# Optimization experiments

Hardware: AMD Instinct MI355X
Metric: run time of the kernel (lower is better)

The kernel has to match this reference:

```python
import jax, jax.numpy as jnp
import numpy as np

LAMDA = 0.5
BATCH_SIZE = 1024
MARGIN = 0.5
NEG_OFFSET = 100000.0
INTRA_MARGIN = 0.1
EPS = 1e-12


def setup_inputs() -> dict:
    key = jax.random.key(0)
    k1, k2, k3 = jax.random.split(key, 3)
    feat = jax.random.normal(k1, (2 * BATCH_SIZE, 128), dtype=jnp.float32)
    label1 = jax.random.randint(k2, (BATCH_SIZE,), 0, 128, dtype=jnp.int64)
    label2 = jax.random.randint(k3, (BATCH_SIZE,), 0, 128, dtype=jnp.int64)
    return {"feat": feat, "label1": label1, "label2": label2}


def _cdist(a, b):
    # faithful to source: broadcasted diff, sqrt(sum(d^2) + 1e-12)
    diffs = a[:, None, :] - b[None, :, :]          # [N, M, D]
    return jnp.sqrt(jnp.sum(diffs * diffs, axis=-1) + EPS)


def _half(f_a, f_b, lab_a, lab_b, f_intra, margin):
    dis = _cdist(f_a, f_b)                          # [B, B]
    s = (lab_a[:, None] == lab_b[None, :]).astype(dis.dtype)
    furthest_positive = jnp.max(dis * s, axis=1)
    pos_positive = jnp.argmax(dis * s, axis=1)
    closest_negative = jnp.min(dis + NEG_OFFSET * s, axis=1)
    pos_negative = jnp.argmin(dis + NEG_OFFSET * s, axis=1)
    cross = jnp.mean(jnp.clip(furthest_positive - closest_negative + margin, 0.0))
    dis_intra = _cdist(f_intra, f_intra)            # [B, B]
    gathered = dis_intra[pos_positive, pos_negative]  # gather_2d equivalent
    intra = jnp.mean(jnp.clip(INTRA_MARGIN - gathered, 0.0))
    return cross, intra


def reference(feat, label1, label2):
    feature1 = feat[:BATCH_SIZE]
    feature2 = feat[BATCH_SIZE:]
    cross1, intra1 = _half(feature1, feature2, label1, label2, feature2, MARGIN)
    cross2, intra2 = _half(feature2, feature1, label2, label1, feature1, MARGIN)
    return (cross1 + cross2) + LAMDA * (intra1 + intra2)
```

## Files before the change

### kernel.cpp

```cpp
#include <hip/hip_runtime.h>
#include <math.h>
#include <float.h>

#define BATCH 1024
#define DIM 128
#define EPSV 1e-12f
#define MARGIN 0.5f
#define INTRA_MARGIN 0.1f
#define LAMDA 0.5f

typedef __attribute__((ext_vector_type(8))) short s16x8;
typedef __attribute__((ext_vector_type(4))) float f32x4;

__device__ __forceinline__ ushort f2bf(float f) {
    unsigned u = __float_as_uint(f);
    return (ushort)((u + 0x7fffu + ((u >> 16) & 1u)) >> 16);
}

__device__ __forceinline__ void gl_lds16(const void* g, void* l) {
    __builtin_amdgcn_global_load_lds(
        (const __attribute__((address_space(1))) unsigned int*)g,
        (__attribute__((address_space(3))) unsigned int*)l,
        16, 0, 0);
}

#define WAITVM4()  do { asm volatile("s_waitcnt vmcnt(4)" ::: "memory"); __builtin_amdgcn_sched_barrier(0); } while (0)
#define WAITVM0()  do { asm volatile("s_waitcnt vmcnt(0)" ::: "memory"); __builtin_amdgcn_sched_barrier(0); } while (0)
#define WAITLGKM() do { asm volatile("s_waitcnt lgkmcnt(0)" ::: "memory"); __builtin_amdgcn_sched_barrier(0); } while (0)

__global__ __launch_bounds__(256) void prep_kernel(
    const float* __restrict__ feat, ushort* __restrict__ bhi,
    float* __restrict__ norm2)
{
    const int t = threadIdx.x;
    const int gt  = blockIdx.x * 256 + t;
    const int row = gt >> 4, seg = gt & 15;
    const float4* p = reinterpret_cast<const float4*>(feat + (size_t)row * DIM + seg * 8);
    const float4 a = p[0], b = p[1];
    const float v[8] = {a.x, a.y, a.z, a.w, b.x, b.y, b.z, b.w};
    ushort h[8];
    float n = 0.0f;
    #pragma unroll
    for (int e = 0; e < 8; ++e) {
        h[e] = f2bf(v[e]);
        n = fmaf(v[e], v[e], n);
    }
    uint4 uh;
    uh.x = (uint)h[0] | ((uint)h[1] << 16); uh.y = (uint)h[2] | ((uint)h[3] << 16);
    uh.z = (uint)h[4] | ((uint)h[5] << 16); uh.w = (uint)h[6] | ((uint)h[7] << 16);
    reinterpret_cast<uint4*>(bhi)[row * 16 + (seg ^ (row & 7))] = uh;
    n += __shfl_xor(n, 1); n += __shfl_xor(n, 2);
    n += __shfl_xor(n, 4); n += __shfl_xor(n, 8);
    if ((t & 15) == 0) norm2[row] = n;
}

__device__ __forceinline__ void issue_chunk(const char* bbytes, size_t gbase,
                                            char* buf, int w, int lane) {
    #pragma unroll
    for (int i = 0; i < 4; ++i) {
        const int o = w * 4096 + i * 1024 + lane * 16;
        gl_lds16(bbytes + gbase + o, buf + o);
    }
}

__global__ __launch_bounds__(512, 2) void gemm_kernel(
    const ushort* __restrict__ bhi, const float* __restrict__ norm2,
    const float* __restrict__ feat,
    const int* __restrict__ label1, const int* __restrict__ label2,
    float* __restrict__ partial)
{
    __shared__ __align__(16) char smem[65536];

    const int rg    = blockIdx.x;
    const int half  = rg >> 7;
    const int arow0 = (rg & 127) * 8;
    const int aglob0 = half * BATCH + arow0;
    const int bglob0 = (half ^ 1) * BATCH;

    const int t = threadIdx.x;
    const int w = t >> 6, lane = t & 63;
    const int l15 = lane & 15, kg = lane >> 4;

    const int* labA = half ? label2 : label1;
    const int* labB = half ? label1 : label2;

    float nb[8]; int lb[8];
    #pragma unroll
    for (int c = 0; c < 8; ++c) {
        const int jc = c * 128 + w * 16 + l15;
        nb[c] = norm2[bglob0 + jc];
        lb[c] = labB[jc];
    }
    float na[4]; int la[4];
    #pragma unroll
    for (int r = 0; r < 4; ++r) {
        const int rr = (kg * 4 + r) & 7;
        na[r] = norm2[aglob0 + rr];
        la[r] = labA[arow0 + rr];
    }

    s16x8 ah[4];
    const size_t abase = (size_t)(aglob0 + (l15 & 7)) * DIM;
    #pragma unroll
    for (int kt = 0; kt < 4; ++kt) {
        const int kh = (kt * 32 + kg * 8) ^ ((l15 & 7) << 3);
        ah[kt] = *reinterpret_cast<const s16x8*>(bhi + abase + kh);
    }

    const char* bbytes = reinterpret_cast<const char*>(bhi);
    char* buf0 = smem;
    char* buf1 = smem + 32768;
    issue_chunk(bbytes, (size_t)(bglob0 + 0 * 128) * 256, buf0, w, lane);
    issue_chunk(bbytes, (size_t)(bglob0 + 1 * 128) * 256, buf1, w, lane);
    WAITVM4();

    float bpv[4], bnv[4]; int bpj[4], bnj[4];
    #pragma unroll
    for (int r = 0; r < 4; ++r) { bpv[r] = -1.0f; bpj[r] = 0x7fffffff; bnv[r] = FLT_MAX; bnj[r] = 0x7fffffff; }

    const int jl = w * 16 + l15;
    const ushort* b0 = reinterpret_cast<const ushort*>(buf0);
    const ushort* b1 = reinterpret_cast<const ushort*>(buf1);

    #pragma unroll
    for (int c = 0; c < 8; ++c) {
        const ushort* bufc = (c & 1) ? b1 : b0;

        s16x8 bh[4];
        #pragma unroll
        for (int kt = 0; kt < 4; ++kt) {
            const int kh = (kt * 32 + kg * 8) ^ ((l15 & 7) << 3);
            bh[kt] = *reinterpret_cast<const s16x8*>(bufc + jl * DIM + kh);
        }
        if (c < 6) {
            WAITLGKM();
            issue_chunk(bbytes, (size_t)(bglob0 + (c + 2) * 128) * 256,
                        (c & 1) ? buf1 : buf0, w, lane);
        }

        f32x4 acc = (f32x4){0.f, 0.f, 0.f, 0.f};
        #pragma unroll
        for (int kt = 0; kt < 4; ++kt)
            acc = __builtin_amdgcn_mfma_f32_16x16x32_bf16(ah[kt], bh[kt], acc, 0, 0, 0);

        const int jc = c * 128 + jl;
        #pragma unroll
        for (int r = 0; r < 4; ++r) {
            const float d2 = fmaxf(na[r] + nb[c] - 2.0f * acc[r], 0.0f);
            const bool same = (la[r] == lb[c]);
            const float pv = same ? d2 : 0.0f;
            const float nv = same ? FLT_MAX : d2;
            if (pv > bpv[r]) { bpv[r] = pv; bpj[r] = jc; }
            if (nv < bnv[r]) { bnv[r] = nv; bnj[r] = jc; }
        }

        if (c < 6)      WAITVM4();
        else if (c == 6) WAITVM0();
    }

    #pragma unroll
    for (int r = 0; r < 4; ++r) {
        #pragma unroll
        for (int m = 8; m > 0; m >>= 1) {
            const float opv = __shfl_xor(bpv[r], m); const int opj = __shfl_xor(bpj[r], m);
            if (opv > bpv[r] || (opv == bpv[r] && opj < bpj[r])) { bpv[r] = opv; bpj[r] = opj; }
            const float onv = __shfl_xor(bnv[r], m); const int onj = __shfl_xor(bnj[r], m);
            if (onv < bnv[r] || (onv == bnv[r] && onj < bnj[r])) { bnv[r] = onv; bnj[r] = onj; }
        }
    }

    __syncthreads();

    float (*L_pv)[8] = (float(*)[8])(smem);
    int   (*L_pj)[8] = (int  (*)[8])(smem + 512);
    float (*L_nv)[8] = (float(*)[8])(smem + 1024);
    int   (*L_nj)[8] = (int  (*)[8])(smem + 1536);
    int*   s_pp = (int*)  (smem + 2048);
    int*   s_pn = (int*)  (smem + 2112);
    float* s_fp = (float*)(smem + 2176);
    float* s_cn = (float*)(smem + 2240);
    float* ls   = (float*)(smem + 2304);

    if (l15 == 0) {
        #pragma unroll
        for (int r = 0; r < 4; ++r) {
            const int rib = kg * 4 + r;
            L_pv[rib][w] = bpv[r]; L_pj[rib][w] = bpj[r];
            L_nv[rib][w] = bnv[r]; L_nj[rib][w] = bnj[r];
        }
    }
    __syncthreads();

    if (t < 8) {
        float pv = -1.0f; int pj = 0x7fffffff; float nv = FLT_MAX; int nj = 0x7fffffff;
        #pragma unroll
        for (int c = 0; c < 8; ++c) {
            const float v1 = L_pv[t][c]; const int j1 = L_pj[t][c];
            if (v1 > pv || (v1 == pv && j1 < pj)) { pv = v1; pj = j1; }
            const float v2 = L_nv[t][c]; const int j2 = L_nj[t][c];
            if (v2 < nv || (v2 == nv && j2 < nj)) { nv = v2; nj = j2; }
        }
        s_pp[t] = pj > (BATCH - 1) ? (BATCH - 1) : pj;
        s_pn[t] = nj > (BATCH - 1) ? (BATCH - 1) : nj;
        s_fp[t] = (pv > 0.0f) ? sqrtf(pv + EPSV) : 0.0f;
        s_cn[t] = sqrtf(nv + EPSV);
    }
    __syncthreads();

    if (t < 128) {
        const int g = t >> 4, sl = t & 15;
        const float* fB = feat + (size_t)(half ^ 1) * BATCH * DIM;
        const float4* x = reinterpret_cast<const float4*>(fB + (size_t)s_pp[g] * DIM + sl * 8);
        const float4* y = reinterpret_cast<const float4*>(fB + (size_t)s_pn[g] * DIM + sl * 8);
        const float4 x0 = x[0], x1 = x[1], y0 = y[0], y1 = y[1];
        float d, d2;
        d = x0.x - y0.x; d2  = d * d;  d = x0.y - y0.y; d2 += d * d;
        d = x0.z - y0.z; d2 += d * d;  d = x0.w - y0.w; d2 += d * d;
        d = x1.x - y1.x; d2 += d * d;  d = x1.y - y1.y; d2 += d * d;
        d = x1.z - y1.z; d2 += d * d;  d = x1.w - y1.w; d2 += d * d;
        d2 += __shfl_xor(d2, 1); d2 += __shfl_xor(d2, 2);
        d2 += __shfl_xor(d2, 4); d2 += __shfl_xor(d2, 8);
        if (sl == 0) {
            const float gd = sqrtf(d2 + EPSV);
            const float loss = fmaxf(s_fp[g] - s_cn[g] + MARGIN, 0.0f)
                             + LAMDA * fmaxf(INTRA_MARGIN - gd, 0.0f);
            ls[g] = loss * (1.0f / (float)BATCH);
        }
    }
    __syncthreads();

    if (t == 0) {
        float s = 0.0f;
        #pragma unroll
        for (int i = 0; i < 8; ++i) s += ls[i];
        partial[rg] = s;
    }
}

__global__ __launch_bounds__(256) void reduce_kernel(
    const float* __restrict__ partial, float* __restrict__ out)
{
    const int t = threadIdx.x;
    float s = partial[t];
    #pragma unroll
    for (int m = 32; m > 0; m >>= 1) s += __shfl_down(s, m);
    __shared__ float ws4[4];
    if ((t & 63) == 0) ws4[t >> 6] = s;
    __syncthreads();
    if (t == 0) out[0] = ws4[0] + ws4[1] + ws4[2] + ws4[3];
}

extern "C" void kernel_launch(void* const* d_in, const int* in_sizes, int n_in,
                              void* d_out, int out_size, void* d_ws, size_t ws_size,
                              hipStream_t stream) {
    const float* feat   = (const float*)d_in[0];
    const int*   label1 = (const int*)d_in[1];
    const int*   label2 = (const int*)d_in[2];
    float* out = (float*)d_out;

    char* ws = (char*)d_ws;
    float*  partial = (float*)(ws);
    ushort* bhi     = (ushort*)(ws + 4096);
    float*  norm2   = (float*)(ws + 4096 + 512 * 1024);

    prep_kernel<<<dim3(128), dim3(256), 0, stream>>>(feat, bhi, norm2);
    gemm_kernel<<<dim3(256), dim3(512), 0, stream>>>(
        bhi, norm2, feat, label1, label2, partial);
    reduce_kernel<<<dim3(1), dim3(256), 0, stream>>>(partial, out);
}
```

Measured before the change: 21.12 us.

## Quad-buffer B chunks in LDS with three-deep prefetch and single-wave reduce

The GEMM kernel now uses four 32KB LDS buffers and keeps three B-chunk loads in flight instead of two, with adjusted vmcnt waits. It also drops the lgkmcnt wait that came before reissuing into a buffer. The intent is to hide more global-load latency. The cost is 128KB of LDS per block, which lowers occupancy to one block per CU (launch bounds changed to 1). The reduce kernel shrinks to a single wave that sums four partials per thread, removing the shared-memory step and the barrier.

After: 20.91 us, median of 2. No clear change (-1.0%).

```diff
diff --git a/kernel.cpp b/kernel.cpp
--- a/kernel.cpp
+++ b/kernel.cpp
@@ -24,9 +24,9 @@
         16, 0, 0);
 }
 
+#define WAITVM8()  do { asm volatile("s_waitcnt vmcnt(8)" ::: "memory"); __builtin_amdgcn_sched_barrier(0); } while (0)
 #define WAITVM4()  do { asm volatile("s_waitcnt vmcnt(4)" ::: "memory"); __builtin_amdgcn_sched_barrier(0); } while (0)
 #define WAITVM0()  do { asm volatile("s_waitcnt vmcnt(0)" ::: "memory"); __builtin_amdgcn_sched_barrier(0); } while (0)
-#define WAITLGKM() do { asm volatile("s_waitcnt lgkmcnt(0)" ::: "memory"); __builtin_amdgcn_sched_barrier(0); } while (0)
 
 __global__ __launch_bounds__(256) void prep_kernel(
     const float* __restrict__ feat, ushort* __restrict__ bhi,
@@ -63,13 +63,13 @@
     }
 }
 
-__global__ __launch_bounds__(512, 2) void gemm_kernel(
+__global__ __launch_bounds__(512, 1) void gemm_kernel(
     const ushort* __restrict__ bhi, const float* __restrict__ norm2,
     const float* __restrict__ feat,
     const int* __restrict__ label1, const int* __restrict__ label2,
     float* __restrict__ partial)
 {
-    __shared__ __align__(16) char smem[65536];
+    __shared__ __align__(16) char smem[131072];
 
     const int rg    = blockIdx.x;
     const int half  = rg >> 7;
@@ -108,23 +108,20 @@
     }
 
     const char* bbytes = reinterpret_cast<const char*>(bhi);
-    char* buf0 = smem;
-    char* buf1 = smem + 32768;
-    issue_chunk(bbytes, (size_t)(bglob0 + 0 * 128) * 256, buf0, w, lane);
-    issue_chunk(bbytes, (size_t)(bglob0 + 1 * 128) * 256, buf1, w, lane);
-    WAITVM4();
+    issue_chunk(bbytes, (size_t)(bglob0 + 0 * 128) * 256, smem + 0 * 32768, w, lane);
+    issue_chunk(bbytes, (size_t)(bglob0 + 1 * 128) * 256, smem + 1 * 32768, w, lane);
+    issue_chunk(bbytes, (size_t)(bglob0 + 2 * 128) * 256, smem + 2 * 32768, w, lane);
+    WAITVM8();
 
     float bpv[4], bnv[4]; int bpj[4], bnj[4];
     #pragma unroll
     for (int r = 0; r < 4; ++r) { bpv[r] = -1.0f; bpj[r] = 0x7fffffff; bnv[r] = FLT_MAX; bnj[r] = 0x7fffffff; }
 
     const int jl = w * 16 + l15;
-    const ushort* b0 = reinterpret_cast<const ushort*>(buf0);
-    const ushort* b1 = reinterpret_cast<const ushort*>(buf1);
 
     #pragma unroll
     for (int c = 0; c < 8; ++c) {
-        const ushort* bufc = (c & 1) ? b1 : b0;
+        const ushort* bufc = reinterpret_cast<const ushort*>(smem + (c & 3) * 32768);
 
         s16x8 bh[4];
         #pragma unroll
@@ -132,11 +129,9 @@
             const int kh = (kt * 32 + kg * 8) ^ ((l15 & 7) << 3);
             bh[kt] = *reinterpret_cast<const s16x8*>(bufc + jl * DIM + kh);
         }
-        if (c < 6) {
-            WAITLGKM();
-            issue_chunk(bbytes, (size_t)(bglob0 + (c + 2) * 128) * 256,
-                        (c & 1) ? buf1 : buf0, w, lane);
-        }
+        if (c <= 4)
+            issue_chunk(bbytes, (size_t)(bglob0 + (c + 3) * 128) * 256,
+                        smem + ((c + 3) & 3) * 32768, w, lane);
 
         f32x4 acc = (f32x4){0.f, 0.f, 0.f, 0.f};
         #pragma unroll
@@ -154,7 +149,8 @@
             if (nv < bnv[r]) { bnv[r] = nv; bnj[r] = jc; }
         }
 
-        if (c < 6)      WAITVM4();
+        if (c <= 4)      WAITVM8();
+        else if (c == 5) WAITVM4();
         else if (c == 6) WAITVM0();
     }
 
@@ -237,17 +233,14 @@
     }
 }
 
-__global__ __launch_bounds__(256) void reduce_kernel(
+__global__ __launch_bounds__(64) void reduce_kernel(
     const float* __restrict__ partial, float* __restrict__ out)
 {
     const int t = threadIdx.x;
-    float s = partial[t];
+    float s = partial[t] + partial[t + 64] + partial[t + 128] + partial[t + 192];
     #pragma unroll
     for (int m = 32; m > 0; m >>= 1) s += __shfl_down(s, m);
-    __shared__ float ws4[4];
-    if ((t & 63) == 0) ws4[t >> 6] = s;
-    __syncthreads();
-    if (t == 0) out[0] = ws4[0] + ws4[1] + ws4[2] + ws4[3];
+    if (t == 0) out[0] = s;
 }
 
 extern "C" void kernel_launch(void* const* d_in, const int* in_sizes, int n_in,
@@ -266,5 +259,5 @@
     prep_kernel<<<dim3(128), dim3(256), 0, stream>>>(feat, bhi, norm2);
     gemm_kernel<<<dim3(256), dim3(512), 0, stream>>>(
         bhi, norm2, feat, label1, label2, partial);
-    reduce_kernel<<<dim3(1), dim3(256), 0, stream>>>(partial, out);
-}
+    reduce_kernel<<<dim3(1), dim3(64), 0, stream>>>(partial, out);
+}
```
